# Kernel optimization log

Measured on AMD Instinct MI355X. Metric: run time of the kernel, lower is better.

The kernel has to match this reference:

```python
import jax, jax.numpy as jnp
import numpy as np

CHANNEL = 64
RATIO = 8
C1 = CHANNEL // RATIO


def setup_inputs() -> dict:
    key = jax.random.key(0)
    ks = jax.random.split(key, 8)
    b, c, h, w = 2, CHANNEL, 96, 96
    X = jax.random.normal(ks[0], (b, c, h, w), dtype=jnp.float32)
    Y = jax.random.normal(ks[1], (b, c, h, w), dtype=jnp.float32)
    # 1x1 conv weights (stored as [out, in]) + biases, Kaiming-ish scale
    s = 1.0 / np.sqrt(c)
    Wq = jax.random.uniform(ks[2], (C1, c), jnp.float32, -s, s)
    bq = jax.random.uniform(ks[3], (C1,), jnp.float32, -s, s)
    Wk = jax.random.uniform(ks[4], (C1, c), jnp.float32, -s, s)
    bk = jax.random.uniform(ks[5], (C1,), jnp.float32, -s, s)
    Wv = jax.random.uniform(ks[6], (c, c), jnp.float32, -s, s)
    bv = jax.random.uniform(ks[7], (c,), jnp.float32, -s, s)
    return {"X": X, "Y": Y, "Wq": Wq, "bq": bq, "Wk": Wk, "bk": bk, "Wv": Wv, "bv": bv}


def reference(X, Y, Wq, bq, Wk, bk, Wv, bv):
    b, c, h, w = Y.shape
    n = h * w
    # 1x1 convs as channel contractions -> [b, n, c_out]
    Xf = X.reshape(b, c, n)                       # [b, c, n]
    q = jnp.einsum('oc,bcn->bno', Wq, Xf) + bq    # [b, n, c1]
    k = jnp.einsum('oc,bcn->bno', Wk, Xf) + bk    # [b, n, c1]
    v = jnp.einsum('oc,bcn->bno', Wv, Y.reshape(b, c, n)) + bv  # [b, n, c]
    scores = jnp.einsum('bic,bjc->bij', q, k)     # [b, n, n]
    # NOTE: softmax over dim=1 (the first n axis), as in the original module
    a = jax.nn.softmax(scores, axis=1)
    x = jnp.einsum('bij,bjc->bic', a, v)          # [b, n, c]
    x = x.transpose(0, 2, 1).reshape(b, c, h, w)
    return Y + x
```

## Files before the change

kernel.cpp:

```cpp
#include <hip/hip_runtime.h>

#define NPOS 9216
#define NB 2
#define CCH 64
#define JSPLIT 8
#define JCHUNK (NPOS / JSPLIT)
#define NSTEP (JCHUNK / 64)

typedef __attribute__((ext_vector_type(8))) short short8;
typedef __attribute__((ext_vector_type(4))) float f32x4;

#define LOG2E 1.4426950408889634f

__device__ __forceinline__ ushort f2bf(float x) {
    unsigned u = __builtin_bit_cast(unsigned, x);
    u += 0x7FFFu + ((u >> 16) & 1u);
    return (ushort)(u >> 16);
}

__device__ __forceinline__ unsigned cvt_pk_bf16(float lo, float hi) {
    unsigned r;
    asm("v_cvt_pk_bf16_f32 %0, %1, %2" : "=v"(r) : "v"(lo), "v"(hi));
    return r;
}

__global__ __launch_bounds__(256) void qkv_kernel(
    const float* __restrict__ X, const float* __restrict__ Y,
    const float* __restrict__ Wq, const float* __restrict__ bq,
    const float* __restrict__ Wk, const float* __restrict__ bk,
    const float* __restrict__ Wv, const float* __restrict__ bv,
    ushort* __restrict__ qb, ushort* __restrict__ kb,
    ushort* __restrict__ vT, float* __restrict__ out)
{
    __shared__ float wqkT[1024];
    __shared__ float wvTs[4096];
    int tid = threadIdx.x;
    for (int idx = tid; idx < 1024; idx += 256) {
        int c = idx >> 4, o = idx & 15;
        wqkT[idx] = (o < 8) ? Wq[o * 64 + c] : Wk[(o - 8) * 64 + c];
    }
    for (int idx = tid; idx < 4096; idx += 256) {
        int c = idx >> 6, o = idx & 63;
        wvTs[idx] = Wv[o * 64 + c];
    }
    __syncthreads();

    int p = tid & 63, s = tid >> 6;
    int base = blockIdx.x * 64;
    int b = base / NPOS;
    int n = (base % NPOS) + p;

    float va[16], qk[8];
    #pragma unroll
    for (int o = 0; o < 16; ++o) va[o] = bv[s * 16 + o];
    #pragma unroll
    for (int o = 0; o < 8; ++o) qk[o] = 0.f;
    if (s == 0) {
        #pragma unroll
        for (int o = 0; o < 8; ++o) qk[o] = bq[o];
    } else if (s == 1) {
        #pragma unroll
        for (int o = 0; o < 8; ++o) qk[o] = bk[o];
    }

    const float* Xb = X + (size_t)b * CCH * NPOS + n;
    const float* Yb = Y + (size_t)b * CCH * NPOS + n;
    float* ob = out + (size_t)b * CCH * NPOS + n;
    for (int c = 0; c < 64; ++c) {
        float yv = Yb[(size_t)c * NPOS];
        ob[(size_t)c * NPOS] = yv;
        const float4* wv4 = (const float4*)(wvTs + c * 64 + s * 16);
        #pragma unroll
        for (int o4 = 0; o4 < 4; ++o4) {
            float4 wv = wv4[o4];
            va[o4*4+0] += wv.x * yv; va[o4*4+1] += wv.y * yv;
            va[o4*4+2] += wv.z * yv; va[o4*4+3] += wv.w * yv;
        }
        if (s < 2) {
            float xv = Xb[(size_t)c * NPOS];
            const float4* wq4 = (const float4*)(wqkT + c * 16 + s * 8);
            float4 w0 = wq4[0], w1 = wq4[1];
            qk[0] += w0.x * xv; qk[1] += w0.y * xv;
            qk[2] += w0.z * xv; qk[3] += w0.w * xv;
            qk[4] += w1.x * xv; qk[5] += w1.y * xv;
            qk[6] += w1.z * xv; qk[7] += w1.w * xv;
        }
    }
    ushort* vdst = vT + (size_t)b * CCH * NPOS + n;
    #pragma unroll
    for (int o = 0; o < 16; ++o)
        vdst[(size_t)(s * 16 + o) * NPOS] = f2bf(va[o]);
    if (s < 2) {
        if (s == 0) {
            #pragma unroll
            for (int o = 0; o < 8; ++o) qk[o] *= LOG2E;
        }
        short8 row;
        #pragma unroll
        for (int o = 0; o < 8; ++o) row[o] = (short)f2bf(qk[o]);
        ushort* dst = (s == 0 ? qb : kb) + ((size_t)b * NPOS + n) * 8;
        *(short8*)dst = row;
    }
}

__global__ __launch_bounds__(256) void zpass_kernel(
    const ushort* __restrict__ qb, const ushort* __restrict__ kb,
    float* __restrict__ Z)
{
    int tid = threadIdx.x;
    int w = tid >> 6, l = tid & 63;
    int il = l & 15, g = l >> 4;
    int b = blockIdx.z;
    int jb = blockIdx.x * 64 + w * 16;
    const short8 zero8 = {0,0,0,0,0,0,0,0};
    const f32x4 cz = {0.f,0.f,0.f,0.f};

    short8 kf = zero8;
    if (g == 0) kf = *(const short8*)(kb + ((size_t)b * NPOS + jb + il) * 8);

    float za[4] = {0.f, 0.f, 0.f, 0.f};
    const ushort* qrow = qb + ((size_t)b * NPOS + blockIdx.y * 2304 + il) * 8;
    #pragma unroll 4
    for (int is = 0; is < 144; ++is) {
        short8 qf = *(const short8*)(qrow + (size_t)is * 128);
        if (g != 0) qf = zero8;
        f32x4 sv = __builtin_amdgcn_mfma_f32_16x16x32_bf16(kf, qf, cz, 0, 0, 0);
        za[0] += __builtin_amdgcn_exp2f(sv[0]);
        za[1] += __builtin_amdgcn_exp2f(sv[1]);
        za[2] += __builtin_amdgcn_exp2f(sv[2]);
        za[3] += __builtin_amdgcn_exp2f(sv[3]);
    }
    #pragma unroll
    for (int r = 0; r < 4; ++r) {
        float x = za[r];
        x += __shfl_xor(x, 1, 16);
        x += __shfl_xor(x, 2, 16);
        x += __shfl_xor(x, 4, 16);
        x += __shfl_xor(x, 8, 16);
        za[r] = x;
    }
    if (il == 0) {
        #pragma unroll
        for (int r = 0; r < 4; ++r)
            atomicAdd(&Z[(size_t)b * NPOS + jb + g * 4 + r], za[r]);
    }
}

__global__ __launch_bounds__(256) void recipz_kernel(
    const float* __restrict__ Z, float* __restrict__ rz)
{
    int i = blockIdx.x * 256 + threadIdx.x;
    rz[i] = __builtin_amdgcn_rcpf(Z[i]);
}

__global__ __launch_bounds__(256) void pass2_kernel(
    const ushort* __restrict__ qb, const ushort* __restrict__ kb,
    const ushort* __restrict__ vT, const float* __restrict__ rz,
    float* __restrict__ out)
{
    __shared__ ushort vz_lds[2][64 * 64];
    __shared__ ushort p_lds[4][32 * 64];
    int tid = threadIdx.x;
    int w = tid >> 6, l = tid & 63;
    int il = l & 15, g = l >> 4;
    int b = blockIdx.z;
    int ibase = blockIdx.x * 128 + w * 32;
    int j0 = blockIdx.y * JCHUNK;

    const short8 zero8 = {0,0,0,0,0,0,0,0};
    const f32x4 cz = {0.f,0.f,0.f,0.f};

    short8 qf0 = zero8, qf1 = zero8;
    if (g == 0) {
        qf0 = *(const short8*)(qb + ((size_t)b * NPOS + ibase + il) * 8);
        qf1 = *(const short8*)(qb + ((size_t)b * NPOS + ibase + 16 + il) * 8);
    }

    f32x4 acc[2][4];
    #pragma unroll
    for (int h = 0; h < 2; ++h)
        #pragma unroll
        for (int cg = 0; cg < 4; ++cg) acc[h][cg] = cz;

    const ushort* kbb = kb + (size_t)b * NPOS * 8;
    const float* rzb = rz + (size_t)b * NPOS;

    int sr = tid >> 2, sq = tid & 3;
    const ushort* vrow = vT + (size_t)b * CCH * NPOS + (size_t)sr * NPOS + j0;
    int soff0 = (sq ^ (sr & 7)) * 8;
    int soff1 = ((sq + 4) ^ (sr & 7)) * 8;
    int xr = il & 7;

    {
        float4 ga = *(const float4*)(vrow + sq * 8);
        float4 gb = *(const float4*)(vrow + (sq + 4) * 8);
        *(float4*)&vz_lds[0][sr * 64 + soff0] = ga;
        *(float4*)&vz_lds[0][sr * 64 + soff1] = gb;
    }
    short8 kf[4];
    #pragma unroll
    for (int t = 0; t < 4; ++t)
        kf[t] = (g == 0) ? *(const short8*)(kbb + (size_t)(j0 + 16 * t + il) * 8)
                         : zero8;
    __syncthreads();

    ushort* pw = p_lds[w];

    for (int st = 0; st < NSTEP; ++st) {
        int jb = j0 + st * 64;
        int cur = st & 1;
        bool more = (st + 1) < NSTEP;

        float4 g0n = {0,0,0,0}, g1n = {0,0,0,0};
        short8 kn[4] = {zero8, zero8, zero8, zero8};
        if (more) {
            int jn = (st + 1) * 64;
            g0n = *(const float4*)(vrow + jn + sq * 8);
            g1n = *(const float4*)(vrow + jn + (sq + 4) * 8);
            #pragma unroll
            for (int t = 0; t < 4; ++t)
                if (g == 0)
                    kn[t] = *(const short8*)(kbb + (size_t)(jb + 64 + 16 * t + il) * 8);
        }
        float4 rzv[4];
        #pragma unroll
        for (int t = 0; t < 4; ++t)
            rzv[t] = *(const float4*)(rzb + jb + 16 * t + 4 * g);

        #pragma unroll
        for (int h = 0; h < 2; ++h) {
            short8 qf = h ? qf1 : qf0;
            int rowoff = (16 * h + il) * 64;
            #pragma unroll
            for (int t = 0; t < 4; ++t) {
                f32x4 sv = __builtin_amdgcn_mfma_f32_16x16x32_bf16(kf[t], qf, cz, 0, 0, 0);
                float p0 = __builtin_amdgcn_exp2f(sv[0]) * rzv[t].x;
                float p1 = __builtin_amdgcn_exp2f(sv[1]) * rzv[t].y;
                float p2 = __builtin_amdgcn_exp2f(sv[2]) * rzv[t].z;
                float p3 = __builtin_amdgcn_exp2f(sv[3]) * rzv[t].w;
                uint2 u;
                u.x = cvt_pk_bf16(p0, p1);
                u.y = cvt_pk_bf16(p2, p3);
                int stored = (2 * t + (g >> 1)) ^ xr;
                *(uint2*)&pw[rowoff + stored * 8 + (g & 1) * 4] = u;
            }
        }

        short8 pf[2][2];
        #pragma unroll
        for (int h = 0; h < 2; ++h) {
            int rowoff = (16 * h + il) * 64;
            pf[h][0] = *(short8*)&pw[rowoff + ((g ^ xr) * 8)];
            pf[h][1] = *(short8*)&pw[rowoff + (((4 + g) ^ xr) * 8)];
        }

        #pragma unroll
        for (int cg = 0; cg < 4; ++cg) {
            int row = (cg * 16 + il) * 64;
            short8 af0 = *(short8*)&vz_lds[cur][row + ((g ^ xr) * 8)];
            short8 af1 = *(short8*)&vz_lds[cur][row + (((4 + g) ^ xr) * 8)];
            #pragma unroll
            for (int h = 0; h < 2; ++h) {
                acc[h][cg] = __builtin_amdgcn_mfma_f32_16x16x32_bf16(af0, pf[h][0], acc[h][cg], 0, 0, 0);
                acc[h][cg] = __builtin_amdgcn_mfma_f32_16x16x32_bf16(af1, pf[h][1], acc[h][cg], 0, 0, 0);
            }
        }

        if (more) {
            *(float4*)&vz_lds[cur ^ 1][sr * 64 + soff0] = g0n;
            *(float4*)&vz_lds[cur ^ 1][sr * 64 + soff1] = g1n;
            #pragma unroll
            for (int t = 0; t < 4; ++t) kf[t] = kn[t];
        }
        __syncthreads();
    }

    float* ob = out + (size_t)b * CCH * NPOS + ibase + il;
    #pragma unroll
    for (int h = 0; h < 2; ++h)
        #pragma unroll
        for (int cg = 0; cg < 4; ++cg)
            #pragma unroll
            for (int r = 0; r < 4; ++r)
                atomicAdd(ob + (size_t)(cg * 16 + g * 4 + r) * NPOS + 16 * h,
                          acc[h][cg][r]);
}

extern "C" void kernel_launch(void* const* d_in, const int* in_sizes, int n_in,
                              void* d_out, int out_size, void* d_ws, size_t ws_size,
                              hipStream_t stream) {
    const float* X  = (const float*)d_in[0];
    const float* Y  = (const float*)d_in[1];
    const float* Wq = (const float*)d_in[2];
    const float* bq = (const float*)d_in[3];
    const float* Wk = (const float*)d_in[4];
    const float* bk = (const float*)d_in[5];
    const float* Wv = (const float*)d_in[6];
    const float* bv = (const float*)d_in[7];

    char* ws = (char*)d_ws;
    ushort* qb  = (ushort*)(ws);
    ushort* kbw = (ushort*)(ws + 294912);
    ushort* vT  = (ushort*)(ws + 589824);
    float*  Z   = (float*) (ws + 2949120);
    float*  rz  = (float*) (ws + 3022848);

    hipMemsetAsync(Z, 0, (size_t)NB * NPOS * sizeof(float), stream);

    qkv_kernel<<<288, 256, 0, stream>>>(X, Y, Wq, bq, Wk, bk, Wv, bv,
                                        qb, kbw, vT, (float*)d_out);
    zpass_kernel<<<dim3(144, 4, NB), 256, 0, stream>>>(qb, kbw, Z);
    recipz_kernel<<<72, 256, 0, stream>>>(Z, rz);
    pass2_kernel<<<dim3(72, JSPLIT, NB), 256, 0, stream>>>(qb, kbw, vT, rz,
                                                           (float*)d_out);
}
```

Measured before the change: 218.9 us.

## Restructure QKV, Z-pass and PV pass with register P fragments and LDS reduction

The QKV projection now uses 32 positions per block with eight channel groups, writing the residual copy once at the end. The column-sum pass switches to 32x32x16 MFMA with prefetched q fragments. The recipz kernel is removed and reciprocals are computed inline in pass2. Pass2 now keeps the softmax probabilities in registers as 16x16x16 MFMA operands instead of round-tripping them through LDS, and splits j across waves with an in-block LDS reduction before the atomics. Together these aim to cut launches, LDS traffic and global atomics, at the cost of more barriers and a different MFMA shape.

```diff
diff --git a/kernel.cpp b/kernel.cpp
--- a/kernel.cpp
+++ b/kernel.cpp
@@ -8,9 +8,19 @@
 #define NSTEP (JCHUNK / 64)
 
 typedef __attribute__((ext_vector_type(8))) short short8;
+typedef __attribute__((ext_vector_type(4))) short short4b;
 typedef __attribute__((ext_vector_type(4))) float f32x4;
+typedef __attribute__((ext_vector_type(16))) float f32x16;
 
 #define LOG2E 1.4426950408889634f
+
+__device__ __forceinline__ f32x4 mfma16(short4b a, short4b b, f32x4 c) {
+#if defined(__HIP_DEVICE_COMPILE__)
+    return __builtin_amdgcn_mfma_f32_16x16x16bf16_1k(a, b, c, 0, 0, 0);
+#else
+    return c;
+#endif
+}
 
 __device__ __forceinline__ ushort f2bf(float x) {
     unsigned u = __builtin_bit_cast(unsigned, x);
@@ -45,14 +55,14 @@
     }
     __syncthreads();
 
-    int p = tid & 63, s = tid >> 6;
-    int base = blockIdx.x * 64;
+    int p = tid & 31, s = tid >> 5;
+    int base = blockIdx.x * 32;
     int b = base / NPOS;
     int n = (base % NPOS) + p;
 
-    float va[16], qk[8];
-    #pragma unroll
-    for (int o = 0; o < 16; ++o) va[o] = bv[s * 16 + o];
+    float va[8], qk[8], ysave[8];
+    #pragma unroll
+    for (int o = 0; o < 8; ++o) va[o] = bv[s * 8 + o];
     #pragma unroll
     for (int o = 0; o < 8; ++o) qk[o] = 0.f;
     if (s == 0) {
@@ -65,31 +75,31 @@
 
     const float* Xb = X + (size_t)b * CCH * NPOS + n;
     const float* Yb = Y + (size_t)b * CCH * NPOS + n;
+    for (int co = 0; co < 8; ++co) {
+        #pragma unroll
+        for (int ci = 0; ci < 8; ++ci) {
+            int c = co * 8 + ci;
+            float yv = Yb[(size_t)c * NPOS];
+            if (co == s) ysave[ci] = yv;
+            const float* wv = wvTs + c * 64 + s * 8;
+            #pragma unroll
+            for (int o = 0; o < 8; ++o) va[o] += wv[o] * yv;
+            if (s < 2) {
+                float xv = Xb[(size_t)c * NPOS];
+                const float* wq = wqkT + c * 16 + s * 8;
+                #pragma unroll
+                for (int o = 0; o < 8; ++o) qk[o] += wq[o] * xv;
+            }
+        }
+    }
+
+    ushort* vdst = vT + (size_t)b * CCH * NPOS + n;
     float* ob = out + (size_t)b * CCH * NPOS + n;
-    for (int c = 0; c < 64; ++c) {
-        float yv = Yb[(size_t)c * NPOS];
-        ob[(size_t)c * NPOS] = yv;
-        const float4* wv4 = (const float4*)(wvTs + c * 64 + s * 16);
-        #pragma unroll
-        for (int o4 = 0; o4 < 4; ++o4) {
-            float4 wv = wv4[o4];
-            va[o4*4+0] += wv.x * yv; va[o4*4+1] += wv.y * yv;
-            va[o4*4+2] += wv.z * yv; va[o4*4+3] += wv.w * yv;
-        }
-        if (s < 2) {
-            float xv = Xb[(size_t)c * NPOS];
-            const float4* wq4 = (const float4*)(wqkT + c * 16 + s * 8);
-            float4 w0 = wq4[0], w1 = wq4[1];
-            qk[0] += w0.x * xv; qk[1] += w0.y * xv;
-            qk[2] += w0.z * xv; qk[3] += w0.w * xv;
-            qk[4] += w1.x * xv; qk[5] += w1.y * xv;
-            qk[6] += w1.z * xv; qk[7] += w1.w * xv;
-        }
-    }
-    ushort* vdst = vT + (size_t)b * CCH * NPOS + n;
-    #pragma unroll
-    for (int o = 0; o < 16; ++o)
-        vdst[(size_t)(s * 16 + o) * NPOS] = f2bf(va[o]);
+    #pragma unroll
+    for (int o = 0; o < 8; ++o) {
+        vdst[(size_t)(s * 8 + o) * NPOS] = f2bf(va[o]);
+        ob[(size_t)(s * 8 + o) * NPOS] = ysave[o];
+    }
     if (s < 2) {
         if (s == 0) {
             #pragma unroll
@@ -109,181 +119,174 @@
 {
     int tid = threadIdx.x;
     int w = tid >> 6, l = tid & 63;
-    int il = l & 15, g = l >> 4;
+    int il2 = l & 31, h = l >> 5;
     int b = blockIdx.z;
-    int jb = blockIdx.x * 64 + w * 16;
+    int jb = blockIdx.x * 128 + w * 32;
+    int i0 = blockIdx.y * 1152;
     const short8 zero8 = {0,0,0,0,0,0,0,0};
-    const f32x4 cz = {0.f,0.f,0.f,0.f};
+    f32x16 cz16;
+    #pragma unroll
+    for (int r = 0; r < 16; ++r) cz16[r] = 0.f;
 
     short8 kf = zero8;
-    if (g == 0) kf = *(const short8*)(kb + ((size_t)b * NPOS + jb + il) * 8);
-
-    float za[4] = {0.f, 0.f, 0.f, 0.f};
-    const ushort* qrow = qb + ((size_t)b * NPOS + blockIdx.y * 2304 + il) * 8;
-    #pragma unroll 4
-    for (int is = 0; is < 144; ++is) {
-        short8 qf = *(const short8*)(qrow + (size_t)is * 128);
-        if (g != 0) qf = zero8;
-        f32x4 sv = __builtin_amdgcn_mfma_f32_16x16x32_bf16(kf, qf, cz, 0, 0, 0);
-        za[0] += __builtin_amdgcn_exp2f(sv[0]);
-        za[1] += __builtin_amdgcn_exp2f(sv[1]);
-        za[2] += __builtin_amdgcn_exp2f(sv[2]);
-        za[3] += __builtin_amdgcn_exp2f(sv[3]);
-    }
-    #pragma unroll
-    for (int r = 0; r < 4; ++r) {
+    if (h == 0) kf = *(const short8*)(kb + ((size_t)b * NPOS + jb + il2) * 8);
+
+    f32x16 za = cz16;
+    const ushort* qrow = qb + ((size_t)b * NPOS + i0 + il2) * 8;
+    short8 qf = (h == 0) ? *(const short8*)qrow : zero8;
+    for (int it = 0; it < 36; ++it) {
+        short8 qn = zero8;
+        if (h == 0 && (it + 1) < 36)
+            qn = *(const short8*)(qrow + (size_t)(it + 1) * 256);
+        f32x16 sv = __builtin_amdgcn_mfma_f32_32x32x16_bf16(kf, qf, cz16, 0, 0, 0);
+        #pragma unroll
+        for (int r = 0; r < 16; ++r) za[r] += __builtin_amdgcn_exp2f(sv[r]);
+        qf = qn;
+    }
+    #pragma unroll
+    for (int r = 0; r < 16; ++r) {
         float x = za[r];
-        x += __shfl_xor(x, 1, 16);
-        x += __shfl_xor(x, 2, 16);
-        x += __shfl_xor(x, 4, 16);
-        x += __shfl_xor(x, 8, 16);
+        x += __shfl_xor(x, 1, 32);
+        x += __shfl_xor(x, 2, 32);
+        x += __shfl_xor(x, 4, 32);
+        x += __shfl_xor(x, 8, 32);
+        x += __shfl_xor(x, 16, 32);
         za[r] = x;
     }
-    if (il == 0) {
-        #pragma unroll
-        for (int r = 0; r < 4; ++r)
-            atomicAdd(&Z[(size_t)b * NPOS + jb + g * 4 + r], za[r]);
-    }
-}
-
-__global__ __launch_bounds__(256) void recipz_kernel(
-    const float* __restrict__ Z, float* __restrict__ rz)
-{
-    int i = blockIdx.x * 256 + threadIdx.x;
-    rz[i] = __builtin_amdgcn_rcpf(Z[i]);
+    if (il2 == 0) {
+        #pragma unroll
+        for (int r = 0; r < 16; ++r) {
+            int j = jb + (r & 3) + 8 * (r >> 2) + 4 * h;
+            atomicAdd(&Z[(size_t)b * NPOS + j], za[r]);
+        }
+    }
 }
 
 __global__ __launch_bounds__(256) void pass2_kernel(
     const ushort* __restrict__ qb, const ushort* __restrict__ kb,
-    const ushort* __restrict__ vT, const float* __restrict__ rz,
+    const ushort* __restrict__ vT, const float* __restrict__ Z,
     float* __restrict__ out)
 {
-    __shared__ ushort vz_lds[2][64 * 64];
-    __shared__ ushort p_lds[4][32 * 64];
+    __shared__ ushort vz[2][64 * 64];
     int tid = threadIdx.x;
     int w = tid >> 6, l = tid & 63;
     int il = l & 15, g = l >> 4;
     int b = blockIdx.z;
-    int ibase = blockIdx.x * 128 + w * 32;
+    int ibase = blockIdx.x * 64;
     int j0 = blockIdx.y * JCHUNK;
+    int jw = w * 16;
 
     const short8 zero8 = {0,0,0,0,0,0,0,0};
     const f32x4 cz = {0.f,0.f,0.f,0.f};
 
-    short8 qf0 = zero8, qf1 = zero8;
-    if (g == 0) {
-        qf0 = *(const short8*)(qb + ((size_t)b * NPOS + ibase + il) * 8);
-        qf1 = *(const short8*)(qb + ((size_t)b * NPOS + ibase + 16 + il) * 8);
-    }
-
-    f32x4 acc[2][4];
-    #pragma unroll
-    for (int h = 0; h < 2; ++h)
-        #pragma unroll
-        for (int cg = 0; cg < 4; ++cg) acc[h][cg] = cz;
+    short8 qf[4];
+    #pragma unroll
+    for (int it = 0; it < 4; ++it) {
+        qf[it] = zero8;
+        if (g == 0)
+            qf[it] = *(const short8*)(qb + ((size_t)b * NPOS + ibase + it * 16 + il) * 8);
+    }
+
+    f32x4 acc[4][4];
+    #pragma unroll
+    for (int cg = 0; cg < 4; ++cg)
+        #pragma unroll
+        for (int it = 0; it < 4; ++it) acc[cg][it] = cz;
 
     const ushort* kbb = kb + (size_t)b * NPOS * 8;
-    const float* rzb = rz + (size_t)b * NPOS;
+    const float* Zb = Z + (size_t)b * NPOS;
 
     int sr = tid >> 2, sq = tid & 3;
     const ushort* vrow = vT + (size_t)b * CCH * NPOS + (size_t)sr * NPOS + j0;
-    int soff0 = (sq ^ (sr & 7)) * 8;
-    int soff1 = ((sq + 4) ^ (sr & 7)) * 8;
-    int xr = il & 7;
+    int so0 = (sq ^ (sr & 7)) * 8;
+    int so1 = ((sq + 4) ^ (sr & 7)) * 8;
 
     {
         float4 ga = *(const float4*)(vrow + sq * 8);
-        float4 gb = *(const float4*)(vrow + (sq + 4) * 8);
-        *(float4*)&vz_lds[0][sr * 64 + soff0] = ga;
-        *(float4*)&vz_lds[0][sr * 64 + soff1] = gb;
-    }
-    short8 kf[4];
-    #pragma unroll
-    for (int t = 0; t < 4; ++t)
-        kf[t] = (g == 0) ? *(const short8*)(kbb + (size_t)(j0 + 16 * t + il) * 8)
-                         : zero8;
+        float4 gb = *(const float4*)(vrow + sq * 8 + 32);
+        *(float4*)&vz[0][sr * 64 + so0] = ga;
+        *(float4*)&vz[0][sr * 64 + so1] = gb;
+    }
+    short8 kf = zero8;
+    if (g == 0) kf = *(const short8*)(kbb + (size_t)(j0 + jw + il) * 8);
+    float4 Zv = *(const float4*)(Zb + j0 + jw + 4 * g);
     __syncthreads();
 
-    ushort* pw = p_lds[w];
+    int rslot = 2 * w + (g >> 1);
+    int rbyte = (g & 1) * 4;
 
     for (int st = 0; st < NSTEP; ++st) {
-        int jb = j0 + st * 64;
         int cur = st & 1;
         bool more = (st + 1) < NSTEP;
 
-        float4 g0n = {0,0,0,0}, g1n = {0,0,0,0};
-        short8 kn[4] = {zero8, zero8, zero8, zero8};
+        float4 ga = {0,0,0,0}, gb = {0,0,0,0}, Zn = {0,0,0,0};
+        short8 kn = zero8;
         if (more) {
             int jn = (st + 1) * 64;
-            g0n = *(const float4*)(vrow + jn + sq * 8);
-            g1n = *(const float4*)(vrow + jn + (sq + 4) * 8);
+            ga = *(const float4*)(vrow + jn + sq * 8);
+            gb = *(const float4*)(vrow + jn + sq * 8 + 32);
+            if (g == 0) kn = *(const short8*)(kbb + (size_t)(j0 + jn + jw + il) * 8);
+            Zn = *(const float4*)(Zb + j0 + jn + jw + 4 * g);
+        }
+
+        f32x4 sv[4];
+        #pragma unroll
+        for (int it = 0; it < 4; ++it)
+            sv[it] = __builtin_amdgcn_mfma_f32_16x16x32_bf16(kf, qf[it], cz, 0, 0, 0);
+
+        float r0 = __builtin_amdgcn_rcpf(Zv.x);
+        float r1 = __builtin_amdgcn_rcpf(Zv.y);
+        float r2 = __builtin_amdgcn_rcpf(Zv.z);
+        float r3 = __builtin_amdgcn_rcpf(Zv.w);
+
+        short4b pf[4];
+        #pragma unroll
+        for (int it = 0; it < 4; ++it) {
+            float p0 = __builtin_amdgcn_exp2f(sv[it][0]) * r0;
+            float p1 = __builtin_amdgcn_exp2f(sv[it][1]) * r1;
+            float p2 = __builtin_amdgcn_exp2f(sv[it][2]) * r2;
+            float p3 = __builtin_amdgcn_exp2f(sv[it][3]) * r3;
+            uint2 u;
+            u.x = cvt_pk_bf16(p0, p1);
+            u.y = cvt_pk_bf16(p2, p3);
+            pf[it] = __builtin_bit_cast(short4b, u);
+        }
+
+        #pragma unroll
+        for (int cg = 0; cg < 4; ++cg) {
+            int row = cg * 16 + il;
+            short4b af = *(short4b*)&vz[cur][row * 64 + ((rslot ^ (row & 7)) * 8) + rbyte];
             #pragma unroll
-            for (int t = 0; t < 4; ++t)
-                if (g == 0)
-                    kn[t] = *(const short8*)(kbb + (size_t)(jb + 64 + 16 * t + il) * 8);
-        }
-        float4 rzv[4];
-        #pragma unroll
-        for (int t = 0; t < 4; ++t)
-            rzv[t] = *(const float4*)(rzb + jb + 16 * t + 4 * g);
-
-        #pragma unroll
-        for (int h = 0; h < 2; ++h) {
-            short8 qf = h ? qf1 : qf0;
-            int rowoff = (16 * h + il) * 64;
-            #pragma unroll
-            for (int t = 0; t < 4; ++t) {
-                f32x4 sv = __builtin_amdgcn_mfma_f32_16x16x32_bf16(kf[t], qf, cz, 0, 0, 0);
-                float p0 = __builtin_amdgcn_exp2f(sv[0]) * rzv[t].x;
-                float p1 = __builtin_amdgcn_exp2f(sv[1]) * rzv[t].y;
-                float p2 = __builtin_amdgcn_exp2f(sv[2]) * rzv[t].z;
-                float p3 = __builtin_amdgcn_exp2f(sv[3]) * rzv[t].w;
-                uint2 u;
-                u.x = cvt_pk_bf16(p0, p1);
-                u.y = cvt_pk_bf16(p2, p3);
-                int stored = (2 * t + (g >> 1)) ^ xr;
-                *(uint2*)&pw[rowoff + stored * 8 + (g & 1) * 4] = u;
-            }
-        }
-
-        short8 pf[2][2];
-        #pragma unroll
-        for (int h = 0; h < 2; ++h) {
-            int rowoff = (16 * h + il) * 64;
-            pf[h][0] = *(short8*)&pw[rowoff + ((g ^ xr) * 8)];
-            pf[h][1] = *(short8*)&pw[rowoff + (((4 + g) ^ xr) * 8)];
-        }
-
-        #pragma unroll
-        for (int cg = 0; cg < 4; ++cg) {
-            int row = (cg * 16 + il) * 64;
-            short8 af0 = *(short8*)&vz_lds[cur][row + ((g ^ xr) * 8)];
-            short8 af1 = *(short8*)&vz_lds[cur][row + (((4 + g) ^ xr) * 8)];
-            #pragma unroll
-            for (int h = 0; h < 2; ++h) {
-                acc[h][cg] = __builtin_amdgcn_mfma_f32_16x16x32_bf16(af0, pf[h][0], acc[h][cg], 0, 0, 0);
-                acc[h][cg] = __builtin_amdgcn_mfma_f32_16x16x32_bf16(af1, pf[h][1], acc[h][cg], 0, 0, 0);
-            }
+            for (int it = 0; it < 4; ++it)
+                acc[cg][it] = mfma16(af, pf[it], acc[cg][it]);
         }
 
         if (more) {
-            *(float4*)&vz_lds[cur ^ 1][sr * 64 + soff0] = g0n;
-            *(float4*)&vz_lds[cur ^ 1][sr * 64 + soff1] = g1n;
-            #pragma unroll
-            for (int t = 0; t < 4; ++t) kf[t] = kn[t];
+            *(float4*)&vz[cur ^ 1][sr * 64 + so0] = ga;
+            *(float4*)&vz[cur ^ 1][sr * 64 + so1] = gb;
+            kf = kn; Zv = Zn;
         }
         __syncthreads();
     }
 
-    float* ob = out + (size_t)b * CCH * NPOS + ibase + il;
-    #pragma unroll
-    for (int h = 0; h < 2; ++h)
-        #pragma unroll
-        for (int cg = 0; cg < 4; ++cg)
-            #pragma unroll
-            for (int r = 0; r < 4; ++r)
-                atomicAdd(ob + (size_t)(cg * 16 + g * 4 + r) * NPOS + 16 * h,
-                          acc[h][cg][r]);
+    float* red = (float*)vz;
+    float* obase = out + (size_t)b * CCH * NPOS + ibase;
+    int i_l = tid >> 2, c0 = (tid & 3) * 4;
+    #pragma unroll
+    for (int cg = 0; cg < 4; ++cg) {
+        #pragma unroll
+        for (int it = 0; it < 4; ++it)
+            *(f32x4*)&red[w * 1024 + (it * 16 + il) * 16 + 4 * g] = acc[cg][it];
+        __syncthreads();
+        f32x4 sum = *(f32x4*)&red[tid * 4];
+        sum += *(f32x4*)&red[1024 + tid * 4];
+        sum += *(f32x4*)&red[2048 + tid * 4];
+        sum += *(f32x4*)&red[3072 + tid * 4];
+        #pragma unroll
+        for (int e = 0; e < 4; ++e)
+            atomicAdd(obase + (size_t)(cg * 16 + c0 + e) * NPOS + i_l, sum[e]);
+        __syncthreads();
+    }
 }
 
 extern "C" void kernel_launch(void* const* d_in, const int* in_sizes, int n_in,
@@ -303,14 +306,12 @@
     ushort* kbw = (ushort*)(ws + 294912);
     ushort* vT  = (ushort*)(ws + 589824);
     float*  Z   = (float*) (ws + 2949120);
-    float*  rz  = (float*) (ws + 3022848);
-
-    hipMemsetAsync(Z, 0, (size_t)NB * NPOS * sizeof(float), stream);
-
-    qkv_kernel<<<288, 256, 0, stream>>>(X, Y, Wq, bq, Wk, bk, Wv, bv,
+
+    (void)hipMemsetAsync(Z, 0, (size_t)NB * NPOS * sizeof(float), stream);
+
+    qkv_kernel<<<576, 256, 0, stream>>>(X, Y, Wq, bq, Wk, bk, Wv, bv,
                                         qb, kbw, vT, (float*)d_out);
-    zpass_kernel<<<dim3(144, 4, NB), 256, 0, stream>>>(qb, kbw, Z);
-    recipz_kernel<<<72, 256, 0, stream>>>(Z, rz);
-    pass2_kernel<<<dim3(72, JSPLIT, NB), 256, 0, stream>>>(qb, kbw, vT, rz,
-                                                           (float*)d_out);
-}
+    zpass_kernel<<<dim3(72, 8, NB), 256, 0, stream>>>(qb, kbw, Z);
+    pass2_kernel<<<dim3(144, JSPLIT, NB), 256, 0, stream>>>(qb, kbw, vT, Z,
+                                                            (float*)d_out);
+}
```

Result: faster. 199.2 us (-9.0%).
